# Optimization experiments

Hardware: AMD Instinct MI355X
Metric: run time of the kernel (lower is better)

Reference implementation:

```python
import jax, jax.numpy as jnp
import numpy as np

EMBED_DIM = 1024
NUM_HEADS = 16
HEAD_DIM = EMBED_DIM // NUM_HEADS
SCALING = HEAD_DIM ** -0.5


def setup_inputs() -> dict:
    key = jax.random.key(0)
    ks = jax.random.split(key, 11)
    B, S, E = 4, 2048, EMBED_DIM
    s = 1.0 / np.sqrt(E)
    return {
        "query": jax.random.normal(ks[0], (B, S, E), jnp.float32),
        "key": jax.random.normal(ks[1], (B, S, E), jnp.float32),
        "value": jax.random.normal(ks[2], (B, S, E), jnp.float32),
        "q_w": jax.random.normal(ks[3], (E, E), jnp.float32) * s,
        "q_b": jax.random.normal(ks[4], (E,), jnp.float32) * 0.01,
        "k_w": jax.random.normal(ks[5], (E, E), jnp.float32) * s,
        "k_b": jax.random.normal(ks[6], (E,), jnp.float32) * 0.01,
        "v_w": jax.random.normal(ks[7], (E, E), jnp.float32) * s,
        "v_b": jax.random.normal(ks[8], (E,), jnp.float32) * 0.01,
        "out_w": jax.random.normal(ks[9], (E, E), jnp.float32) * s,
        "out_b": jax.random.normal(ks[10], (E,), jnp.float32) * 0.01,
    }


def reference(query, key, value, q_w, q_b, k_w, k_b, v_w, v_b, out_w, out_b):
    B, S, E = query.shape
    H, D = NUM_HEADS, HEAD_DIM
    # torch Linear: x @ W.T + b
    q = (query @ q_w.T + q_b).reshape(B, S, H, D).transpose(0, 2, 1, 3)  # [B,H,S,D]
    k = (key @ k_w.T + k_b).reshape(B, -1, H, D).transpose(0, 2, 1, 3)
    v = (value @ v_w.T + v_b).reshape(B, -1, H, D).transpose(0, 2, 1, 3)
    attn_scores = jnp.einsum("bhsd,bhtd->bhst", q, k) * SCALING  # [B,H,S,S]
    attn_weights = jax.nn.softmax(attn_scores, axis=-1)
    attn_output = jnp.einsum("bhst,bhtd->bhsd", attn_weights, v)
    attn_output = attn_output.transpose(0, 2, 1, 3).reshape(B, S, E)
    return attn_output @ out_w.T + out_b
```

## Files before the change

kernel.cpp:

```cpp
#include <hip/hip_runtime.h>
#include <stdint.h>
#include <stddef.h>

#define BB 4
#define SS 2048
#define EE 1024
#define HH 16
#define DD 64
#define MTOT (BB * SS)

#define SOFTMAX_C (0.125f * 1.44269504088896340736f)

using bf16x8 = __attribute__((ext_vector_type(8))) __bf16;
using f32x4  = __attribute__((ext_vector_type(4))) float;
using s16x4  = __attribute__((ext_vector_type(4))) short;

__device__ inline unsigned short f2bf(float f) {
    union { float f; uint32_t u; } v; v.f = f;
    uint32_t u = v.u;
    u += 0x7fffu + ((u >> 16) & 1u);
    return (unsigned short)(u >> 16);
}

__device__ inline uint32_t packbf_trunc(float lo, float hi) {
    union { float f; uint32_t u; } a, b; a.f = lo; b.f = hi;
    return (a.u >> 16) | (b.u & 0xFFFF0000u);
}

__device__ inline void gld_lds16(const unsigned short* g, unsigned short* l) {
    __builtin_amdgcn_global_load_lds(
        (const __attribute__((address_space(1))) unsigned int*)g,
        (__attribute__((address_space(3))) unsigned int*)l,
        16, 0, 0);
}

__global__ __launch_bounds__(256) void cast3_f32_bf16(
    const float* __restrict__ a, const float* __restrict__ b,
    const float* __restrict__ c,
    unsigned short* __restrict__ oa, unsigned short* __restrict__ ob,
    unsigned short* __restrict__ oc, int n4) {
    int i = blockIdx.x * 256 + threadIdx.x;
    const float* src = (blockIdx.y == 0) ? a : (blockIdx.y == 1) ? b : c;
    unsigned short* dst = (blockIdx.y == 0) ? oa : (blockIdx.y == 1) ? ob : oc;
    if (i < n4) {
        float4 f = ((const float4*)src)[i];
        ushort4 o;
        o.x = f2bf(f.x); o.y = f2bf(f.y); o.z = f2bf(f.z); o.w = f2bf(f.w);
        ((ushort4*)dst)[i] = o;
    }
}

__global__ __launch_bounds__(256) void cast4_f32_bf16(
    const float* __restrict__ a, const float* __restrict__ b,
    const float* __restrict__ c, const float* __restrict__ d,
    unsigned short* __restrict__ oa, unsigned short* __restrict__ ob,
    unsigned short* __restrict__ oc, unsigned short* __restrict__ od, int n4) {
    int i = blockIdx.x * 256 + threadIdx.x;
    const float* src = (blockIdx.y == 0) ? a : (blockIdx.y == 1) ? b
                     : (blockIdx.y == 2) ? c : d;
    unsigned short* dst = (blockIdx.y == 0) ? oa : (blockIdx.y == 1) ? ob
                        : (blockIdx.y == 2) ? oc : od;
    if (i < n4) {
        float4 f = ((const float4*)src)[i];
        ushort4 o;
        o.x = f2bf(f.x); o.y = f2bf(f.y); o.z = f2bf(f.z); o.w = f2bf(f.w);
        ((ushort4*)dst)[i] = o;
    }
}

template <int MODE>
__global__ __launch_bounds__(256) void gemm_nt(
    const unsigned short* __restrict__ A,
    const unsigned short* __restrict__ W,
    const float* __restrict__ bias,
    void* __restrict__ outp, float oscale) {
    __shared__ __align__(16) unsigned short Smem[32768];

    const int tid  = threadIdx.x;
    const int lane = tid & 63;
    const int wid  = tid >> 6;
    const int wm   = wid >> 1;
    const int wn   = wid & 1;
    const int quad = lane >> 4;
    const int l16  = lane & 15;
    const int m0   = blockIdx.y * 128;
    const int n0   = blockIdx.x * 128;

    f32x4 acc[4][4];
#pragma unroll
    for (int i = 0; i < 4; i++)
#pragma unroll
        for (int j = 0; j < 4; j++) acc[i][j] = (f32x4){0.f, 0.f, 0.f, 0.f};

    const int lrow = lane >> 3;
    const int lcol = (lane & 7) * 8;
    const unsigned short* ga = A + (size_t)(m0 + wid * 32 + lrow) * 1024 + lcol;
    const unsigned short* gb = W + (size_t)(n0 + wid * 32 + lrow) * 1024 + lcol;

    auto STAGE = [&](int buf, int k0) {
        unsigned short* la = Smem + buf * 16384 + wid * 32 * 64;
        unsigned short* lb = la + 8192;
#pragma unroll
        for (int c = 0; c < 4; c++) {
            gld_lds16(ga + (size_t)c * 8 * 1024 + k0, la + c * 8 * 64);
            gld_lds16(gb + (size_t)c * 8 * 1024 + k0, lb + c * 8 * 64);
        }
    };

    STAGE(0, 0);
    __syncthreads();

    for (int t = 0; t < 16; ++t) {
        const int cur = t & 1;
        if (t < 15) STAGE(cur ^ 1, (t + 1) * 64);
        const unsigned short* As = Smem + cur * 16384;
        const unsigned short* Bs = As + 8192;
#pragma unroll
        for (int kt = 0; kt < 2; kt++) {
            bf16x8 a[4], b[4];
#pragma unroll
            for (int mt = 0; mt < 4; mt++)
                a[mt] = *(const bf16x8*)(As + (wm * 64 + mt * 16 + l16) * 64 + kt * 32 + quad * 8);
#pragma unroll
            for (int nt = 0; nt < 4; nt++)
                b[nt] = *(const bf16x8*)(Bs + (wn * 64 + nt * 16 + l16) * 64 + kt * 32 + quad * 8);
#pragma unroll
            for (int mt = 0; mt < 4; mt++)
#pragma unroll
                for (int nt = 0; nt < 4; nt++)
                    acc[mt][nt] = __builtin_amdgcn_mfma_f32_16x16x32_bf16(
                        a[mt], b[nt], acc[mt][nt], 0, 0, 0);
        }
        __syncthreads();
    }

    if (MODE == 0 || MODE == 3) {
        constexpr int OS = 136;
        unsigned short* Os = Smem;
#pragma unroll
        for (int mt = 0; mt < 4; mt++)
#pragma unroll
            for (int nt = 0; nt < 4; nt++) {
                int cl = wn * 64 + nt * 16 + l16;
                float bvn = (MODE == 0) ? bias[n0 + cl] : 0.f;
#pragma unroll
                for (int r = 0; r < 4; r++) {
                    int rl = wm * 64 + mt * 16 + quad * 4 + r;
                    float bv = (MODE == 3) ? bias[m0 + rl] : bvn;
                    Os[rl * OS + cl] = f2bf((acc[mt][nt][r] + bv) * oscale);
                }
            }
        __syncthreads();
        if (MODE == 0) {
#pragma unroll
            for (int i = 0; i < 8; i++) {
                int c = tid + 256 * i;
                int row = c >> 4, g = c & 15;
                *(uint4*)((unsigned short*)outp + (size_t)(m0 + row) * 1024 + n0 + g * 8)
                    = *(const uint4*)(Os + row * OS + g * 8);
            }
        } else {
            const int bb = n0 >> 11, s0 = n0 & 2047;
#pragma unroll
            for (int i = 0; i < 8; i++) {
                int c = tid + 256 * i;
                int row = c >> 4, g = c & 15;
                int hh = (m0 + row) >> 6, dd = (m0 + row) & 63;
                *(uint4*)((unsigned short*)outp + (((size_t)(bb * HH + hh)) * DD + dd) * SS + s0 + g * 8)
                    = *(const uint4*)(Os + row * OS + g * 8);
            }
        }
    } else {
#pragma unroll
        for (int mt = 0; mt < 4; mt++)
#pragma unroll
            for (int nt = 0; nt < 4; nt++) {
                int gcol = n0 + wn * 64 + nt * 16 + l16;
                float bvn = bias[gcol];
#pragma unroll
                for (int r = 0; r < 4; r++) {
                    int grow = m0 + wm * 64 + mt * 16 + quad * 4 + r;
                    ((float*)outp)[(size_t)grow * 1024 + gcol] =
                        (acc[mt][nt][r] + bvn) * oscale;
                }
            }
    }
}

__global__ __launch_bounds__(256) void flash_attn6(
    const unsigned short* __restrict__ Qh,
    const unsigned short* __restrict__ Kh,
    const unsigned short* __restrict__ Vtg,
    unsigned short* __restrict__ attn) {
    constexpr int LSK = 72;
    constexpr int LSV = 76;
    constexpr int BUFSZ = 64 * LSK + 64 * LSV;
    constexpr int NT = SS / 64;
    __shared__ __align__(16) unsigned short Sh[2 * BUFSZ];

    const int tid  = threadIdx.x;
    const int lane = tid & 63;
    const int w    = tid >> 6;
    const int quad = lane >> 4;
    const int l16  = lane & 15;
    const int bh   = blockIdx.y;
    const int q0   = blockIdx.x * 128;
    const int b    = bh >> 4, h = bh & 15;
    const size_t baseqk = (size_t)b * SS * EE + h * 64;
    const size_t basev  = (size_t)bh * SS * DD;

    union { unsigned short u[4]; s16x4 v; } onesu;
#pragma unroll
    for (int i = 0; i < 4; i++) onesu.u[i] = 0x3F80;
    const s16x4 ones = onesu.v;

    bf16x8 bq[2][2];
#pragma unroll
    for (int s = 0; s < 2; s++)
#pragma unroll
        for (int kt = 0; kt < 2; kt++)
            bq[s][kt] = *(const bf16x8*)(Qh + baseqk +
                (size_t)(q0 + w * 32 + s * 16 + l16) * EE + kt * 32 + quad * 8);

    f32x4 oT[2][4];
    f32x4 lacc[2];
#pragma unroll
    for (int s = 0; s < 2; s++) {
        lacc[s] = (f32x4){0.f, 0.f, 0.f, 0.f};
#pragma unroll
        for (int dt = 0; dt < 4; dt++) oT[s][dt] = (f32x4){0.f, 0.f, 0.f, 0.f};
    }

    const int crow = tid >> 3;
    const int ccol = (tid & 7) * 8;
    uint4 kreg[2], vreg[2];

    auto LOADT = [&](int j0) {
#pragma unroll
        for (int i = 0; i < 2; ++i) {
            kreg[i] = *(const uint4*)(Kh + baseqk + (size_t)(j0 + crow + 32 * i) * EE + ccol);
            vreg[i] = *(const uint4*)(Vtg + basev + (size_t)(crow + 32 * i) * SS + j0 + ccol);
        }
    };
    auto STORET = [&](unsigned short* KsD, unsigned short* VsD) {
#pragma unroll
        for (int i = 0; i < 2; ++i) {
            int row = crow + 32 * i;
            *(uint4*)(KsD + row * LSK + ccol) = kreg[i];
            *(uint2*)(VsD + row * LSV + ccol)     = uint2{vreg[i].x, vreg[i].y};
            *(uint2*)(VsD + row * LSV + ccol + 4) = uint2{vreg[i].z, vreg[i].w};
        }
    };

    auto COMPUTE = [&](const unsigned short* Ks, const unsigned short* Vs) {
        f32x4 sacc[2][4];
#pragma unroll
        for (int s = 0; s < 2; s++)
#pragma unroll
            for (int mt = 0; mt < 4; mt++) sacc[s][mt] = (f32x4){0.f, 0.f, 0.f, 0.f};
        __builtin_amdgcn_s_setprio(1);
#pragma unroll
        for (int kt = 0; kt < 2; kt++) {
            bf16x8 ak[4];
#pragma unroll
            for (int mt = 0; mt < 4; mt++)
                ak[mt] = *(const bf16x8*)(Ks + (mt * 16 + l16) * LSK + kt * 32 + quad * 8);
#pragma unroll
            for (int s = 0; s < 2; s++)
#pragma unroll
                for (int mt = 0; mt < 4; mt++)
                    sacc[s][mt] = __builtin_amdgcn_mfma_f32_16x16x32_bf16(
                        ak[mt], bq[s][kt], sacc[s][mt], 0, 0, 0);
        }
        __builtin_amdgcn_s_setprio(0);

        s16x4 bpf[2][4];
#pragma unroll
        for (int s = 0; s < 2; s++) {
#pragma unroll
            for (int mt = 0; mt < 4; mt++) {
                float p0 = __builtin_amdgcn_exp2f(sacc[s][mt][0]);
                float p1 = __builtin_amdgcn_exp2f(sacc[s][mt][1]);
                float p2 = __builtin_amdgcn_exp2f(sacc[s][mt][2]);
                float p3 = __builtin_amdgcn_exp2f(sacc[s][mt][3]);
                union { uint32_t w[2]; s16x4 v; } pk;
                pk.w[0] = packbf_trunc(p0, p1);
                pk.w[1] = packbf_trunc(p2, p3);
                bpf[s][mt] = pk.v;
                lacc[s] = __builtin_amdgcn_mfma_f32_16x16x16bf16_1k(
                    ones, pk.v, lacc[s], 0, 0, 0);
            }
        }

        __builtin_amdgcn_s_setprio(1);
#pragma unroll
        for (int mt = 0; mt < 4; mt++) {
#pragma unroll
            for (int dt = 0; dt < 4; dt++) {
                s16x4 av = *(const s16x4*)(Vs + (dt * 16 + l16) * LSV + mt * 16 + quad * 4);
#pragma unroll
                for (int s = 0; s < 2; s++)
                    oT[s][dt] = __builtin_amdgcn_mfma_f32_16x16x16bf16_1k(
                        av, bpf[s][mt], oT[s][dt], 0, 0, 0);
            }
        }
        __builtin_amdgcn_s_setprio(0);
    };

    LOADT(0);
    STORET(Sh, Sh + 64 * LSK);
    __syncthreads();

    for (int jt = 0; jt < NT - 1; ++jt) {
        const int cur = jt & 1;
        const unsigned short* Ks = Sh + cur * BUFSZ;
        LOADT((jt + 1) * 64);
        COMPUTE(Ks, Ks + 64 * LSK);
        unsigned short* Kn = Sh + (cur ^ 1) * BUFSZ;
        STORET(Kn, Kn + 64 * LSK);
        __syncthreads();
    }
    {
        const unsigned short* Ks = Sh + ((NT - 1) & 1) * BUFSZ;
        COMPUTE(Ks, Ks + 64 * LSK);
    }

    float inv_l[2];
#pragma unroll
    for (int s = 0; s < 2; s++) inv_l[s] = 1.f / lacc[s][0];

    __syncthreads();
#pragma unroll
    for (int s = 0; s < 2; s++)
#pragma unroll
        for (int dt = 0; dt < 4; dt++)
#pragma unroll
            for (int r = 0; r < 4; r++)
                Sh[(w * 32 + s * 16 + l16) * LSK + dt * 16 + quad * 4 + r] =
                    f2bf(oT[s][dt][r] * inv_l[s]);
    __syncthreads();

#pragma unroll
    for (int i = 0; i < 4; i++) {
        int c = tid + 256 * i;
        int row = c >> 3, col8 = (c & 7) * 8;
        *(uint4*)(attn + ((size_t)b * SS + q0 + row) * EE + h * 64 + col8) =
            *(const uint4*)(Sh + row * LSK + col8);
    }
}

extern "C" void kernel_launch(void* const* d_in, const int* in_sizes, int n_in,
                              void* d_out, int out_size, void* d_ws, size_t ws_size,
                              hipStream_t stream) {
    (void)in_sizes; (void)n_in; (void)out_size; (void)ws_size;
    const float* q_in  = (const float*)d_in[0];
    const float* k_in  = (const float*)d_in[1];
    const float* v_in  = (const float*)d_in[2];
    const float* q_w   = (const float*)d_in[3];
    const float* q_b   = (const float*)d_in[4];
    const float* k_w   = (const float*)d_in[5];
    const float* k_b   = (const float*)d_in[6];
    const float* v_w   = (const float*)d_in[7];
    const float* v_b   = (const float*)d_in[8];
    const float* out_w = (const float*)d_in[9];
    const float* out_b = (const float*)d_in[10];

    const size_t NX = (size_t)MTOT * EE;
    const size_t NW = (size_t)EE * EE;

    unsigned short* xq = (unsigned short*)d_ws;
    unsigned short* xk = xq + NX;
    unsigned short* xv = xk + NX;
    unsigned short* wq = xv + NX;
    unsigned short* wk = wq + NW;
    unsigned short* wv = wk + NW;
    unsigned short* wo = wv + NW;
    unsigned short* qh = wo + NW;
    unsigned short* kh = qh + NX;
    unsigned short* vt = kh + NX;
    unsigned short* attn = vt + NX;

    cast3_f32_bf16<<<dim3((int)(NX / 4 / 256), 3), 256, 0, stream>>>(
        q_in, k_in, v_in, xq, xk, xv, (int)(NX / 4));
    cast4_f32_bf16<<<dim3((int)(NW / 4 / 256), 4), 256, 0, stream>>>(
        q_w, k_w, v_w, out_w, wq, wk, wv, wo, (int)(NW / 4));

    dim3 ggrid(EE / 128, MTOT / 128);
    dim3 ggridT(MTOT / 128, EE / 128);
    gemm_nt<0><<<ggrid, 256, 0, stream>>>(xq, wq, q_b, qh, SOFTMAX_C);
    gemm_nt<0><<<ggrid, 256, 0, stream>>>(xk, wk, k_b, kh, 1.0f);
    gemm_nt<3><<<ggridT, 256, 0, stream>>>(wv, xv, v_b, vt, 1.0f);

    flash_attn6<<<dim3(SS / 128, BB * HH), 256, 0, stream>>>(qh, kh, vt, attn);

    gemm_nt<1><<<ggrid, 256, 0, stream>>>(attn, wo, out_b, (float*)d_out, 1.0f);
}
```

Before: 383.5 us.

## Merge QKV GEMMs into one launch and single-buffer LDS to raise occupancy

Folds the three QKV projection GEMMs into one kernel launch indexed by blockIdx.z. LDS use drops from 64KB to 32KB per block by removing double buffering and writing the epilogue in two 64-row passes, so more blocks can reside per CU. The grid mapping also changes so blockIdx.x walks M instead of N. The trade-off is that global-to-LDS loads are no longer overlapped with MFMA compute inside a block and each k-step needs extra barriers, so latency hiding now depends on running more blocks at once.

```diff
diff --git a/kernel.cpp b/kernel.cpp
--- a/kernel.cpp
+++ b/kernel.cpp
@@ -69,12 +69,12 @@
 }
 
 template <int MODE>
-__global__ __launch_bounds__(256) void gemm_nt(
+__device__ __forceinline__ void gemm_core(
     const unsigned short* __restrict__ A,
     const unsigned short* __restrict__ W,
     const float* __restrict__ bias,
-    void* __restrict__ outp, float oscale) {
-    __shared__ __align__(16) unsigned short Smem[32768];
+    void* __restrict__ outp, float oscale,
+    int m0, int n0, unsigned short* Smem) {
 
     const int tid  = threadIdx.x;
     const int lane = tid & 63;
@@ -83,8 +83,6 @@
     const int wn   = wid & 1;
     const int quad = lane >> 4;
     const int l16  = lane & 15;
-    const int m0   = blockIdx.y * 128;
-    const int n0   = blockIdx.x * 128;
 
     f32x4 acc[4][4];
 #pragma unroll
@@ -96,25 +94,20 @@
     const int lcol = (lane & 7) * 8;
     const unsigned short* ga = A + (size_t)(m0 + wid * 32 + lrow) * 1024 + lcol;
     const unsigned short* gb = W + (size_t)(n0 + wid * 32 + lrow) * 1024 + lcol;
-
-    auto STAGE = [&](int buf, int k0) {
-        unsigned short* la = Smem + buf * 16384 + wid * 32 * 64;
-        unsigned short* lb = la + 8192;
+    unsigned short* la = Smem + wid * 2048;
+    unsigned short* lb = la + 8192;
+
+    for (int k0 = 0; k0 < 1024; k0 += 64) {
+        __syncthreads();
 #pragma unroll
         for (int c = 0; c < 4; c++) {
-            gld_lds16(ga + (size_t)c * 8 * 1024 + k0, la + c * 8 * 64);
-            gld_lds16(gb + (size_t)c * 8 * 1024 + k0, lb + c * 8 * 64);
-        }
-    };
-
-    STAGE(0, 0);
-    __syncthreads();
-
-    for (int t = 0; t < 16; ++t) {
-        const int cur = t & 1;
-        if (t < 15) STAGE(cur ^ 1, (t + 1) * 64);
-        const unsigned short* As = Smem + cur * 16384;
-        const unsigned short* Bs = As + 8192;
+            gld_lds16(ga + (size_t)c * 8 * 1024 + k0, la + c * 512);
+            gld_lds16(gb + (size_t)c * 8 * 1024 + k0, lb + c * 512);
+        }
+        __syncthreads();
+
+        const unsigned short* As = Smem;
+        const unsigned short* Bs = Smem + 8192;
 #pragma unroll
         for (int kt = 0; kt < 2; kt++) {
             bf16x8 a[4], b[4];
@@ -131,43 +124,49 @@
                     acc[mt][nt] = __builtin_amdgcn_mfma_f32_16x16x32_bf16(
                         a[mt], b[nt], acc[mt][nt], 0, 0, 0);
         }
-        __syncthreads();
     }
 
     if (MODE == 0 || MODE == 3) {
         constexpr int OS = 136;
         unsigned short* Os = Smem;
 #pragma unroll
-        for (int mt = 0; mt < 4; mt++)
-#pragma unroll
-            for (int nt = 0; nt < 4; nt++) {
-                int cl = wn * 64 + nt * 16 + l16;
-                float bvn = (MODE == 0) ? bias[n0 + cl] : 0.f;
-#pragma unroll
-                for (int r = 0; r < 4; r++) {
-                    int rl = wm * 64 + mt * 16 + quad * 4 + r;
-                    float bv = (MODE == 3) ? bias[m0 + rl] : bvn;
-                    Os[rl * OS + cl] = f2bf((acc[mt][nt][r] + bv) * oscale);
+        for (int p = 0; p < 2; ++p) {
+            __syncthreads();
+            if (wm == p) {
+#pragma unroll
+                for (int mt = 0; mt < 4; mt++)
+#pragma unroll
+                    for (int nt = 0; nt < 4; nt++) {
+                        int cl = wn * 64 + nt * 16 + l16;
+                        float bvn = (MODE == 0) ? bias[n0 + cl] : 0.f;
+#pragma unroll
+                        for (int r = 0; r < 4; r++) {
+                            int rl = mt * 16 + quad * 4 + r;
+                            float bv = (MODE == 3) ? bias[m0 + p * 64 + rl] : bvn;
+                            Os[rl * OS + cl] = f2bf((acc[mt][nt][r] + bv) * oscale);
+                        }
+                    }
+            }
+            __syncthreads();
+            if (MODE == 0) {
+#pragma unroll
+                for (int i = 0; i < 4; i++) {
+                    int c = tid + 256 * i;
+                    int row = c >> 4, g = c & 15;
+                    *(uint4*)((unsigned short*)outp + (size_t)(m0 + p * 64 + row) * 1024 + n0 + g * 8)
+                        = *(const uint4*)(Os + row * OS + g * 8);
                 }
-            }
-        __syncthreads();
-        if (MODE == 0) {
-#pragma unroll
-            for (int i = 0; i < 8; i++) {
-                int c = tid + 256 * i;
-                int row = c >> 4, g = c & 15;
-                *(uint4*)((unsigned short*)outp + (size_t)(m0 + row) * 1024 + n0 + g * 8)
-                    = *(const uint4*)(Os + row * OS + g * 8);
-            }
-        } else {
-            const int bb = n0 >> 11, s0 = n0 & 2047;
-#pragma unroll
-            for (int i = 0; i < 8; i++) {
-                int c = tid + 256 * i;
-                int row = c >> 4, g = c & 15;
-                int hh = (m0 + row) >> 6, dd = (m0 + row) & 63;
-                *(uint4*)((unsigned short*)outp + (((size_t)(bb * HH + hh)) * DD + dd) * SS + s0 + g * 8)
-                    = *(const uint4*)(Os + row * OS + g * 8);
+            } else {
+                const int bb = n0 >> 11, s0 = n0 & 2047;
+#pragma unroll
+                for (int i = 0; i < 4; i++) {
+                    int c = tid + 256 * i;
+                    int row = c >> 4, g = c & 15;
+                    int er = m0 + p * 64 + row;
+                    int hh = er >> 6, dd = er & 63;
+                    *(uint4*)((unsigned short*)outp + (((size_t)(bb * HH + hh)) * DD + dd) * SS + s0 + g * 8)
+                        = *(const uint4*)(Os + row * OS + g * 8);
+                }
             }
         }
     } else {
@@ -185,6 +184,32 @@
                 }
             }
     }
+}
+
+__global__ __launch_bounds__(256) void gemm_qkv(
+    const unsigned short* __restrict__ xq, const unsigned short* __restrict__ wq,
+    const float* __restrict__ qb,
+    const unsigned short* __restrict__ xk, const unsigned short* __restrict__ wk,
+    const float* __restrict__ kb,
+    const unsigned short* __restrict__ wv, const unsigned short* __restrict__ xv,
+    const float* __restrict__ vb,
+    unsigned short* __restrict__ qh, unsigned short* __restrict__ kh,
+    unsigned short* __restrict__ vt) {
+    __shared__ __align__(16) unsigned short Smem[16384];
+    const int z = blockIdx.z;
+    if (z == 0)
+        gemm_core<0>(xq, wq, qb, qh, SOFTMAX_C, blockIdx.x * 128, blockIdx.y * 128, Smem);
+    else if (z == 1)
+        gemm_core<0>(xk, wk, kb, kh, 1.0f, blockIdx.x * 128, blockIdx.y * 128, Smem);
+    else
+        gemm_core<3>(wv, xv, vb, vt, 1.0f, blockIdx.y * 128, blockIdx.x * 128, Smem);
+}
+
+__global__ __launch_bounds__(256) void gemm_out(
+    const unsigned short* __restrict__ A, const unsigned short* __restrict__ W,
+    const float* __restrict__ bias, float* __restrict__ outp) {
+    __shared__ __align__(16) unsigned short Smem[16384];
+    gemm_core<1>(A, W, bias, outp, 1.0f, blockIdx.x * 128, blockIdx.y * 128, Smem);
 }
 
 __global__ __launch_bounds__(256) void flash_attn6(
@@ -385,13 +410,10 @@
     cast4_f32_bf16<<<dim3((int)(NW / 4 / 256), 4), 256, 0, stream>>>(
         q_w, k_w, v_w, out_w, wq, wk, wv, wo, (int)(NW / 4));
 
-    dim3 ggrid(EE / 128, MTOT / 128);
-    dim3 ggridT(MTOT / 128, EE / 128);
-    gemm_nt<0><<<ggrid, 256, 0, stream>>>(xq, wq, q_b, qh, SOFTMAX_C);
-    gemm_nt<0><<<ggrid, 256, 0, stream>>>(xk, wk, k_b, kh, 1.0f);
-    gemm_nt<3><<<ggridT, 256, 0, stream>>>(wv, xv, v_b, vt, 1.0f);
+    gemm_qkv<<<dim3(64, 8, 3), 256, 0, stream>>>(
+        xq, wq, q_b, xk, wk, k_b, wv, xv, v_b, qh, kh, vt);
 
     flash_attn6<<<dim3(SS / 128, BB * HH), 256, 0, stream>>>(qh, kh, vt, attn);
 
-    gemm_nt<1><<<ggrid, 256, 0, stream>>>(attn, wo, out_b, (float*)d_out, 1.0f);
-}
+    gemm_out<<<dim3(64, 8), 256, 0, stream>>>(attn, wo, out_b, (float*)d_out);
+}
```

New measurement: 382.7 us. Within noise of the previous version (-0.2%).
